# Optimization experiments

Measured on AMD Instinct MI355X. Metric: run time of the kernel, lower is better.

The kernel has to match this reference:

```python
import jax, jax.numpy as jnp
import numpy as np

B, S, D = 1, 2048, 2048
H = 16            # num query heads
QL = 1536         # q_lora_rank
KVL = 512         # kv_lora_rank
DN = 128          # qk_nope_head_dim
DR = 64           # qk_rope_head_dim
DV = 128          # v_head_dim
F = 8192          # ffn intermediate
EPS = 1e-6
WAVE = 10000.0


def _rms(x, scale, eps=EPS):
    # fp32 norm then cast back, matching DeepSeekV3_1RMSNorm
    x32 = x.astype(jnp.float32)
    ms = jnp.mean(x32 * x32, axis=-1, keepdims=True)
    return (x32 * jax.lax.rsqrt(ms + eps)).astype(x.dtype) * scale


def _rope_tables(seq_len, dim):
    inv_freq = 1.0 / (WAVE ** (jnp.arange(0, dim, 2, dtype=jnp.float32) / dim))
    t = jnp.arange(seq_len, dtype=jnp.float32)[:, None] * inv_freq[None, :]  # [S, dim/2]
    emb = jnp.concatenate([t, t], axis=-1)  # [S, dim]
    return jnp.cos(emb), jnp.sin(emb)


def _apply_rope(x, cos, sin):
    # x: [B, S, H, dr]; rotate-half convention
    half = x.shape[-1] // 2
    x1, x2 = x[..., :half], x[..., half:]
    rot = jnp.concatenate([-x2, x1], axis=-1)
    return x * cos[None, :, None, :] + rot * sin[None, :, None, :]


def setup_inputs() -> dict:
    key = jax.random.key(0)
    ks = jax.random.split(key, 12)
    w = lambda k, shp: (jax.random.normal(k, shp, dtype=jnp.float32) * 0.02)
    inp = {
        "hidden_states": jax.random.normal(ks[0], (B, S, D), dtype=jnp.float32),
        "attention_mask": jnp.broadcast_to(jnp.tril(jnp.ones((S, S), dtype=bool)), (B, S, S)),
        "pre_attn_scale": jnp.ones((D,), jnp.float32),
        "wqa": w(ks[1], (D, QL)),
        "q_norm_scale": jnp.ones((QL,), jnp.float32),
        "wqb": w(ks[2], (QL, H * (DN + DR))),
        "wkva": w(ks[3], (D, KVL + DR)),
        "kv_norm_scale": jnp.ones((KVL,), jnp.float32),
        "wkvb": w(ks[4], (KVL, H * (DN + DV))),
        "wo": w(ks[5], (H * DV, D)),
        "pre_ffn_scale": jnp.ones((D,), jnp.float32),
        "wg": w(ks[6], (D, F)),
        "bg": jnp.zeros((F,), jnp.float32),
        "wu": w(ks[7], (D, F)),
        "bu": jnp.zeros((F,), jnp.float32),
        "wd": w(ks[8], (F, D)),
        "bd": jnp.zeros((D,), jnp.float32),
    }
    return inp


def reference(hidden_states, attention_mask, pre_attn_scale, wqa, q_norm_scale, wqb,
              wkva, kv_norm_scale, wkvb, wo, pre_ffn_scale, wg, bg, wu, bu, wd, bd):
    x = hidden_states
    # --- pre-attention RMSNorm ---
    n = _rms(x, pre_attn_scale)
    # --- MLA attention ---
    q = (_rms(n @ wqa, q_norm_scale) @ wqb).reshape(B, S, H, DN + DR)
    q_nope, q_rope = q[..., :DN], q[..., DN:]
    kva = n @ wkva                              # [B,S,KVL+DR]
    c_kv, k_rope = kva[..., :KVL], kva[..., KVL:]
    kv = (_rms(c_kv, kv_norm_scale) @ wkvb).reshape(B, S, H, DN + DV)
    k_nope, v = kv[..., :DN], kv[..., DN:]
    cos, sin = _rope_tables(S, DR)
    q_rope = _apply_rope(q_rope, cos, sin)
    k_rope = _apply_rope(k_rope[:, :, None, :], cos, sin)  # [B,S,1,DR] shared across heads
    qf = jnp.concatenate([q_nope, q_rope], axis=-1)
    kf = jnp.concatenate([k_nope, jnp.broadcast_to(k_rope, (B, S, H, DR))], axis=-1)
    scale = 1.0 / float(np.sqrt(DN + DR))
    scores = jnp.einsum('bqhd,bkhd->bhqk', qf, kf) * scale
    scores = jnp.where(attention_mask[:, None, :, :], scores, jnp.float32(-1e9))
    probs = jax.nn.softmax(scores, axis=-1)
    attn = jnp.einsum('bhqk,bkhd->bqhd', probs, v).reshape(B, S, H * DV)
    x = x + attn @ wo                            # residual 1 (dropout=0)
    # --- pre-FFN RMSNorm + dense SwiGLU FFN ---
    n = _rms(x, pre_ffn_scale)
    ff = (jax.nn.silu(n @ wg + bg) * (n @ wu + bu)) @ wd + bd
    return x + ff                                # residual 2
```

## Files before the change

kernel.cpp:

```cpp
#include <hip/hip_runtime.h>
#include <hip/hip_bf16.h>
#include <stdint.h>

typedef unsigned short u16;
using f32x4  = __attribute__((ext_vector_type(4))) float;
using bf16x8 = __attribute__((ext_vector_type(8))) __bf16;
using u32x4  = __attribute__((ext_vector_type(4))) uint32_t;
using u16x4  = __attribute__((ext_vector_type(4))) unsigned short;
using u16x8  = __attribute__((ext_vector_type(8))) unsigned short;

#define S_LEN 2048
#define DM    2048
#define NH    16
#define QLR   1536
#define KVLR  512
#define DNOPE 128
#define DROPE 64
#define DVAL  128
#define FFD   8192

static __device__ __forceinline__ float bf2f(u16 u) {
    union { uint32_t i; float f; } v; v.i = ((uint32_t)u) << 16; return v.f;
}
static __device__ __forceinline__ u16 f2bf(float f) {
    union { float f; uint32_t i; } v; v.f = f;
    uint32_t x = v.i;
    return (u16)((x + 0x7FFF + ((x >> 16) & 1)) >> 16);
}
static __device__ __forceinline__ void gload16(const u16* g, const u16* l) {
    __builtin_amdgcn_global_load_lds(
        (const __attribute__((address_space(1))) void*)g,
        (__attribute__((address_space(3))) void*)l, 16, 0, 0);
}

struct TWJob { const float* src; u16* dst; int R, C, xt, start; };
struct TWJobs { TWJob j[4]; };

__global__ __launch_bounds__(256)
void transpose_all(TWJobs jobs)
{
    __shared__ __align__(16) u16 tile[64][68];
    const int bid = blockIdx.x;
    int e = 0;
#pragma unroll
    for (int i = 1; i < 4; ++i) e = (bid >= jobs.j[i].start) ? i : e;
    const float* src = jobs.j[e].src;
    u16* dst = jobs.j[e].dst;
    const int R = jobs.j[e].R, C = jobs.j[e].C;
    const int local = bid - jobs.j[e].start;
    const int c0 = (local % jobs.j[e].xt) * 64;
    const int r0 = (local / jobs.j[e].xt) * 64;
    const int t = threadIdx.x;
#pragma unroll
    for (int i = 0; i < 4; ++i) {
        int idx = i * 256 + t;
        int r = idx >> 4, c4 = idx & 15;
        float4 v = *reinterpret_cast<const float4*>(&src[(size_t)(r0 + r) * C + c0 + c4 * 4]);
        u16x4 b; b[0] = f2bf(v.x); b[1] = f2bf(v.y); b[2] = f2bf(v.z); b[3] = f2bf(v.w);
        *reinterpret_cast<u16x4*>(&tile[r][c4 * 4]) = b;
    }
    __syncthreads();
#pragma unroll
    for (int i = 0; i < 4; ++i) {
        int idx = i * 256 + t;
        int rr = idx >> 4, k4 = idx & 15;
        u16x4 o;
#pragma unroll
        for (int j = 0; j < 4; ++j) o[j] = tile[k4 * 4 + j][rr];
        *reinterpret_cast<u16x4*>(&dst[(size_t)(c0 + rr) * R + r0 + k4 * 4]) = o;
    }
}

__global__ __launch_bounds__(256)
void transpose_v(const u16* __restrict__ kv, u16* __restrict__ vt)
{
    __shared__ __align__(16) u16 tile[64][76];
    const int t = threadIdx.x;
    const int s0 = blockIdx.x * 64;
    const int d0 = blockIdx.y * 64;
    const int h  = blockIdx.z;
#pragma unroll
    for (int i = 0; i < 2; ++i) {
        int idx = i * 256 + t;
        int s = idx >> 3, c8 = idx & 7;
        u16x8 v = *reinterpret_cast<const u16x8*>(kv + (size_t)(s0 + s) * (NH * 256) + h * 256 + 128 + d0 + c8 * 8);
        u16x4 lo, hi;
#pragma unroll
        for (int j = 0; j < 4; ++j) { lo[j] = v[j]; hi[j] = v[4 + j]; }
        *reinterpret_cast<u16x4*>(&tile[s][c8 * 8])     = lo;
        *reinterpret_cast<u16x4*>(&tile[s][c8 * 8 + 4]) = hi;
    }
    __syncthreads();
#pragma unroll
    for (int i = 0; i < 4; ++i) {
        int idx = i * 256 + t;
        int d = idx >> 4, s4 = idx & 15;
        u16x4 o;
#pragma unroll
        for (int j = 0; j < 4; ++j) o[j] = tile[s4 * 4 + j][d];
        *reinterpret_cast<u16x4*>(&vt[(size_t)(h * 128 + d0 + d) * S_LEN + s0 + s4 * 4]) = o;
    }
}

template<bool IN_F32>
__global__ __launch_bounds__(256)
void rms_norm(const void* __restrict__ in, int in_stride, int width,
              const float* __restrict__ scale, u16* __restrict__ out, int out_stride)
{
    const int row = blockIdx.x;
    const int t = threadIdx.x;
    const float* inf = (const float*)in;
    const u16*   inb = (const u16*)in;
    float ss = 0.f;
    for (int c = t; c < width; c += 256) {
        float v = IN_F32 ? inf[(size_t)row * in_stride + c] : bf2f(inb[(size_t)row * in_stride + c]);
        ss += v * v;
    }
#pragma unroll
    for (int o = 32; o > 0; o >>= 1) ss += __shfl_xor(ss, o);
    __shared__ float red[4];
    if ((t & 63) == 0) red[t >> 6] = ss;
    __syncthreads();
    float inv = rsqrtf((red[0] + red[1] + red[2] + red[3]) / (float)width + 1e-6f);
    for (int c = t; c < width; c += 256) {
        float v = IN_F32 ? inf[(size_t)row * in_stride + c] : bf2f(inb[(size_t)row * in_stride + c]);
        out[(size_t)row * out_stride + c] = f2bf(v * inv * scale[c]);
    }
}

__global__ __launch_bounds__(256)
void rope_qk(u16* __restrict__ q, const float* __restrict__ kva, u16* __restrict__ kr)
{
    const int s = blockIdx.x;
    const int t = threadIdx.x;
    for (int idx = t; idx < 544; idx += 256) {
        int d = idx & 31;
        float invf = powf(10000.f, -(float)(2 * d) / 64.f);
        float ang = (float)s * invf;
        float cs = cosf(ang), sn = sinf(ang);
        if (idx < 512) {
            int hh = idx >> 5;
            u16* base = q + ((size_t)s * NH + hh) * 192 + 128;
            float x1 = bf2f(base[d]), x2 = bf2f(base[d + 32]);
            base[d]      = f2bf(x1 * cs - x2 * sn);
            base[d + 32] = f2bf(x2 * cs + x1 * sn);
        } else {
            const float* kb = kva + (size_t)s * 576 + 512;
            float x1 = kb[d], x2 = kb[d + 32];
            kr[(size_t)s * 64 + d]      = f2bf(x1 * cs - x2 * sn);
            kr[(size_t)s * 64 + d + 32] = f2bf(x2 * cs + x1 * sn);
        }
    }
}

__global__ __launch_bounds__(256)
void init_out(const float* __restrict__ x2, const float* __restrict__ bd,
              float* __restrict__ out, int total4, int N)
{
    int i = blockIdx.x * 256 + threadIdx.x;
    const int stride = gridDim.x * 256;
    for (; i < total4; i += stride) {
        float4 r = ((const float4*)x2)[i];
        int col = (i * 4) & (N - 1);
        float4 b = *reinterpret_cast<const float4*>(&bd[col]);
        float4 o; o.x = r.x + b.x; o.y = r.y + b.y; o.z = r.z + b.z; o.w = r.w + b.w;
        ((float4*)out)[i] = o;
    }
}

__global__ __launch_bounds__(256)
void mul_gu(const u16* __restrict__ g, const u16* __restrict__ u,
            u16* __restrict__ h, int total8)
{
    int i = blockIdx.x * 256 + threadIdx.x;
    const int stride = gridDim.x * 256;
    for (; i < total8; i += stride) {
        u16x8 gv = ((const u16x8*)g)[i];
        u16x8 uv = ((const u16x8*)u)[i];
        u16x8 hv;
#pragma unroll
        for (int j = 0; j < 8; ++j) hv[j] = f2bf(bf2f(gv[j]) * bf2f(uv[j]));
        ((u16x8*)h)[i] = hv;
    }
}

struct GJob { const u16* A; const u16* BT; void* out; int N, K, yCount, zCount; };

template<int EPI>
__global__ __launch_bounds__(256)
void gemm_bt2(GJob j0, GJob j1)
{
    __shared__ __align__(16) u16 As[128 * 64];
    __shared__ __align__(16) u16 Bs[128 * 64];
    const int t = threadIdx.x;
    const int lane = t & 63;
    const int w = t >> 6;
    const int wr = w >> 1, wc = w & 1;
    const int li = lane & 15;
    const int lg = lane >> 4;

    const int gx = gridDim.x;
    int nwg = gx * gridDim.y;
    int bid = blockIdx.y * gx + blockIdx.x;
    bid = (bid & 7) * (nwg >> 3) + (bid >> 3);
    const int m0 = (bid % gx) * 128;
    int yy = bid / gx;

    const int j0span = j0.yCount * j0.zCount;
    const GJob& J = (yy < j0span) ? j0 : j1;
    if (yy >= j0span) yy -= j0span;
    const int ntile = yy % J.yCount;
    const int z = yy / J.yCount;
    const int n0 = ntile * 128;
    const int N = J.N, K = J.K;

    const int nktt = K >> 6;
    const int nz = J.zCount;
    const int qq = nktt / nz, rr = nktt % nz;
    const int kt0 = z * qq + (z < rr ? z : rr);
    const int ktEnd = kt0 + qq + (z < rr ? 1 : 0);

    const int srow = w * 32 + (lane >> 3);
    const int scol = (((lane & 7) ^ (lane >> 3)) << 3);
    const u16* ag = J.A  + (size_t)(m0 + srow) * K + scol;
    const u16* bg = J.BT + (size_t)(n0 + srow) * K + scol;

    f32x4 acc[4][4];
#pragma unroll
    for (int m = 0; m < 4; ++m)
#pragma unroll
        for (int n = 0; n < 4; ++n)
            acc[m][n] = f32x4{0.f, 0.f, 0.f, 0.f};

    for (int kt = kt0; kt < ktEnd; ++kt) {
        const int k0 = kt << 6;
        __syncthreads();
#pragma unroll
        for (int i = 0; i < 4; ++i) {
            gload16(ag + (size_t)i * 8 * K + k0, As + (w * 32 + i * 8) * 64);
            gload16(bg + (size_t)i * 8 * K + k0, Bs + (w * 32 + i * 8) * 64);
        }
        __syncthreads();
#pragma unroll
        for (int kk = 0; kk < 2; ++kk) {
            const int csw = (kk * 32 + lg * 8) ^ ((li & 7) << 3);
            bf16x8 af[4], bfr[4];
#pragma unroll
            for (int m = 0; m < 4; ++m)
                af[m] = *reinterpret_cast<const bf16x8*>(As + (wr * 64 + m * 16 + li) * 64 + csw);
#pragma unroll
            for (int n = 0; n < 4; ++n)
                bfr[n] = *reinterpret_cast<const bf16x8*>(Bs + (wc * 64 + n * 16 + li) * 64 + csw);
#pragma unroll
            for (int m = 0; m < 4; ++m)
#pragma unroll
                for (int n = 0; n < 4; ++n)
                    acc[m][n] = __builtin_amdgcn_mfma_f32_16x16x32_bf16(af[m], bfr[n], acc[m][n], 0, 0, 0);
        }
    }

#pragma unroll
    for (int m = 0; m < 4; ++m) {
        const int row = m0 + wr * 64 + m * 16 + lg * 4;
#pragma unroll
        for (int n = 0; n < 4; ++n) {
            const int col = n0 + wc * 64 + n * 16 + li;
            if (col < N) {
#pragma unroll
                for (int r2 = 0; r2 < 4; ++r2) {
                    float v = acc[m][n][r2];
                    size_t idx = (size_t)(row + r2) * N + col;
                    if (EPI == 0) ((u16*)J.out)[idx] = f2bf(v);
                    else          unsafeAtomicAdd((float*)J.out + idx, v);
                }
            }
        }
    }
}

template<int EPI>
__global__ __launch_bounds__(512, 4)
void gemm_big(const u16* __restrict__ A, const u16* __restrict__ BT,
              void* __restrict__ out, int M, int N, int K,
              const float* __restrict__ bias, const u16* __restrict__ gmul)
{
    __shared__ __align__(16) u16 As[256 * 64];
    __shared__ __align__(16) u16 Bs[128 * 64];
    const int t = threadIdx.x;
    const int lane = t & 63;
    const int w = t >> 6;
    const int wr = w >> 1, wc = w & 1;
    const int li = lane & 15;
    const int lg = lane >> 4;

    const int gx = gridDim.x;
    int nwg = gx * gridDim.y;
    int bid = blockIdx.y * gx + blockIdx.x;
    bid = (bid & 7) * (nwg >> 3) + (bid >> 3);
    const int m0 = (bid % gx) * 256;
    const int n0 = (bid / gx) * 128;

    const int nz = gridDim.z, z = blockIdx.z;
    const int nktt = K >> 6;
    const int qq = nktt / nz, rr = nktt % nz;
    const int kt0 = z * qq + (z < rr ? z : rr);
    const int ktEnd = kt0 + qq + (z < rr ? 1 : 0);

    const int sr = lane >> 3;
    const int scol = (((lane & 7) ^ sr) << 3);
    const u16* ag = A  + (size_t)(m0 + w * 8 + sr) * K + scol;
    const u16* bg = BT + (size_t)(n0 + w * 8 + sr) * K + scol;
    const u16* lA = As + (w * 8) * 64;
    const u16* lB = Bs + (w * 8) * 64;

    f32x4 acc[4][4];
#pragma unroll
    for (int m = 0; m < 4; ++m)
#pragma unroll
        for (int n = 0; n < 4; ++n)
            acc[m][n] = f32x4{0.f, 0.f, 0.f, 0.f};

    for (int kt = kt0; kt < ktEnd; ++kt) {
        const int k0 = kt << 6;
        __syncthreads();
#pragma unroll
        for (int i = 0; i < 4; ++i)
            gload16(ag + (size_t)i * 64 * K + k0, lA + i * 64 * 64);
#pragma unroll
        for (int i = 0; i < 2; ++i)
            gload16(bg + (size_t)i * 64 * K + k0, lB + i * 64 * 64);
        __syncthreads();
        __builtin_amdgcn_s_setprio(1);
#pragma unroll
        for (int kk = 0; kk < 2; ++kk) {
            const int csw = (kk * 32 + lg * 8) ^ ((li & 7) << 3);
            bf16x8 af[4], bfr[4];
#pragma unroll
            for (int m = 0; m < 4; ++m)
                af[m] = *reinterpret_cast<const bf16x8*>(As + (wr * 64 + m * 16 + li) * 64 + csw);
#pragma unroll
            for (int n = 0; n < 4; ++n)
                bfr[n] = *reinterpret_cast<const bf16x8*>(Bs + (wc * 64 + n * 16 + li) * 64 + csw);
#pragma unroll
            for (int m = 0; m < 4; ++m)
#pragma unroll
                for (int n = 0; n < 4; ++n)
                    acc[m][n] = __builtin_amdgcn_mfma_f32_16x16x32_bf16(af[m], bfr[n], acc[m][n], 0, 0, 0);
        }
        __builtin_amdgcn_s_setprio(0);
    }

#pragma unroll
    for (int m = 0; m < 4; ++m) {
        const int row = m0 + wr * 64 + m * 16 + lg * 4;
#pragma unroll
        for (int n = 0; n < 4; ++n) {
            const int col = n0 + wc * 64 + n * 16 + li;
#pragma unroll
            for (int r2 = 0; r2 < 4; ++r2) {
                float v = acc[m][n][r2];
                size_t idx = (size_t)(row + r2) * N + col;
                if (EPI == 0) {
                    ((u16*)out)[idx] = f2bf(v);
                } else if (EPI == 1) {
                    v += bias[col];
                    v = v / (1.f + __expf(-v));
                    ((u16*)out)[idx] = f2bf(v);
                } else {
                    unsafeAtomicAdd((float*)out + idx, v);
                }
            }
        }
    }
}

__global__ __launch_bounds__(512, 4)
void gemm_gu(const u16* __restrict__ A, const u16* __restrict__ BgT, const u16* __restrict__ BuT,
             u16* __restrict__ gout, u16* __restrict__ uout, int M, int N, int K,
             const float* __restrict__ bg, const float* __restrict__ bu)
{
    __shared__ __align__(16) u16 As[256 * 64];
    __shared__ __align__(16) u16 Bs[128 * 64];
    const int t = threadIdx.x;
    const int lane = t & 63;
    const int w = t >> 6;
    const int wr = w >> 1, wc = w & 1;
    const int li = lane & 15;
    const int lg = lane >> 4;
    const int isUp = blockIdx.z;

    const u16* BT = isUp ? BuT : BgT;
    const float* bias = isUp ? bu : bg;
    u16* out = isUp ? uout : gout;

    const int gx = gridDim.x;
    int nwg = gx * gridDim.y;
    int bid = blockIdx.y * gx + blockIdx.x;
    bid = (bid & 7) * (nwg >> 3) + (bid >> 3);
    const int m0 = (bid % gx) * 256;
    const int n0 = (bid / gx) * 128;

    const int sr = lane >> 3;
    const int scol = (((lane & 7) ^ sr) << 3);
    const u16* ag = A  + (size_t)(m0 + w * 8 + sr) * K + scol;
    const u16* bgp = BT + (size_t)(n0 + w * 8 + sr) * K + scol;
    const u16* lA = As + (w * 8) * 64;
    const u16* lB = Bs + (w * 8) * 64;

    f32x4 acc[4][4];
#pragma unroll
    for (int m = 0; m < 4; ++m)
#pragma unroll
        for (int n = 0; n < 4; ++n)
            acc[m][n] = f32x4{0.f, 0.f, 0.f, 0.f};

    const int nkt = K >> 6;
    for (int kt = 0; kt < nkt; ++kt) {
        const int k0 = kt << 6;
        __syncthreads();
#pragma unroll
        for (int i = 0; i < 4; ++i)
            gload16(ag + (size_t)i * 64 * K + k0, lA + i * 64 * 64);
#pragma unroll
        for (int i = 0; i < 2; ++i)
            gload16(bgp + (size_t)i * 64 * K + k0, lB + i * 64 * 64);
        __syncthreads();
        __builtin_amdgcn_s_setprio(1);
#pragma unroll
        for (int kk = 0; kk < 2; ++kk) {
            const int csw = (kk * 32 + lg * 8) ^ ((li & 7) << 3);
            bf16x8 af[4], bfr[4];
#pragma unroll
            for (int m = 0; m < 4; ++m)
                af[m] = *reinterpret_cast<const bf16x8*>(As + (wr * 64 + m * 16 + li) * 64 + csw);
#pragma unroll
            for (int n = 0; n < 4; ++n)
                bfr[n] = *reinterpret_cast<const bf16x8*>(Bs + (wc * 64 + n * 16 + li) * 64 + csw);
#pragma unroll
            for (int m = 0; m < 4; ++m)
#pragma unroll
                for (int n = 0; n < 4; ++n)
                    acc[m][n] = __builtin_amdgcn_mfma_f32_16x16x32_bf16(af[m], bfr[n], acc[m][n], 0, 0, 0);
        }
        __builtin_amdgcn_s_setprio(0);
    }

#pragma unroll
    for (int m = 0; m < 4; ++m) {
        const int row = m0 + wr * 64 + m * 16 + lg * 4;
#pragma unroll
        for (int n = 0; n < 4; ++n) {
            const int col = n0 + wc * 64 + n * 16 + li;
            float bv = bias[col];
#pragma unroll
            for (int r2 = 0; r2 < 4; ++r2) {
                float v = acc[m][n][r2] + bv;
                if (!isUp) v = v / (1.f + __expf(-v));
                ((u16*)out)[(size_t)(row + r2) * N + col] = f2bf(v);
            }
        }
    }
}

struct TW4 { const float* src; u16* dst; int R, C, xt, gstart; };
struct TW4s { TW4 j[4]; };

__global__ __launch_bounds__(512)
void attn_tw(const u16* __restrict__ q, const u16* __restrict__ kv,
             const u16* __restrict__ kr, const u16* __restrict__ vt,
             u16* __restrict__ attn, TW4s tj)
{
    __shared__ __align__(16) u16 SMEM[2 * 20480 + 8 * 16 * 72];

    if (blockIdx.y >= 16) {
        u16 (*tile)[68] = reinterpret_cast<u16(*)[68]>(SMEM);
        const int g = (blockIdx.y - 16) * 16 + blockIdx.x;
        int e = 0;
#pragma unroll
        for (int i = 1; i < 4; ++i) e = (g >= tj.j[i].gstart) ? i : e;
        const float* src = tj.j[e].src;
        u16* dst = tj.j[e].dst;
        const int R = tj.j[e].R, C = tj.j[e].C, xt = tj.j[e].xt;
        const int base = (g - tj.j[e].gstart) * 8;
        const int t = threadIdx.x;
        for (int ti = 0; ti < 8; ++ti) {
            const int local = base + ti;
            const int c0 = (local % xt) * 64;
            const int r0 = (local / xt) * 64;
            __syncthreads();
#pragma unroll
            for (int i = 0; i < 2; ++i) {
                int idx = i * 512 + t;
                int r = idx >> 4, c4 = idx & 15;
                float4 v = *reinterpret_cast<const float4*>(&src[(size_t)(r0 + r) * C + c0 + c4 * 4]);
                u16x4 b; b[0] = f2bf(v.x); b[1] = f2bf(v.y); b[2] = f2bf(v.z); b[3] = f2bf(v.w);
                *reinterpret_cast<u16x4*>(&tile[r][c4 * 4]) = b;
            }
            __syncthreads();
#pragma unroll
            for (int i = 0; i < 2; ++i) {
                int idx = i * 512 + t;
                int rr = idx >> 4, k4 = idx & 15;
                u16x4 o;
#pragma unroll
                for (int j = 0; j < 4; ++j) o[j] = tile[k4 * 4 + j][rr];
                *reinterpret_cast<u16x4*>(&dst[(size_t)(c0 + rr) * R + r0 + k4 * 4]) = o;
            }
        }
        return;
    }

    u16 (*KVs)[20480] = reinterpret_cast<u16(*)[20480]>(SMEM);
    u16 (*Ps)[16][72] = reinterpret_cast<u16(*)[16][72]>(SMEM + 2 * 20480);

    const int t = threadIdx.x;
    const int lane = t & 63;
    const int w = t >> 6;
    const int li = lane & 15;
    const int lg = lane >> 4;
    const int h = blockIdx.x;
    const int b = 15 - blockIdx.y;

    const int qt = (w < 4) ? (2 * b + 1) : (2 * b);
    const int my_nkt = qt + 1;
    const int block_nkt = 2 * b + 2;
    const int wl = w & 3;
    const int qr = qt * 64 + wl * 16;
    const int qpos = qr + li;

    auto stage = [&](int buf, int k0) {
        u16* base = &KVs[buf][0];
#pragma unroll
        for (int i = 0; i < 3; ++i) {
            int g = w * 3 + i;
            int P = g * 64 + lane;
            int j = P / 24, s = P % 24;
            int c = (s & 24) | ((s ^ (j & 7)) & 7);
            const u16* src = (c < 16)
                ? kv + (size_t)(k0 + j) * (NH * 256) + h * 256 + c * 8
                : kr + (size_t)(k0 + j) * 64 + (c - 16) * 8;
            gload16(src, base + g * 512);
        }
#pragma unroll
        for (int i = 0; i < 2; ++i) {
            int g = w * 2 + i;
            int P = g * 64 + lane;
            int d = P >> 3, s8 = P & 7;
            int c = s8 ^ (d & 7);
            const u16* src = vt + (size_t)(h * 128 + d) * S_LEN + k0 + c * 8;
            gload16(src, base + 12288 + g * 512);
        }
    };

    bf16x8 qf[6];
#pragma unroll
    for (int kb = 0; kb < 6; ++kb)
        qf[kb] = *reinterpret_cast<const bf16x8*>(q + ((size_t)(qr + li) * NH + h) * 192 + kb * 32 + lg * 8);

    f32x4 oacc[8];
#pragma unroll
    for (int i = 0; i < 8; ++i) oacc[i] = f32x4{0.f, 0.f, 0.f, 0.f};
    float m_run = -INFINITY, l_run = 0.f;

    stage(0, 0);
    int buf = 0;
    const float scale = 0.07216878364870322f;

    for (int kt = 0; kt < block_nkt; ++kt) {
        const int k0 = kt << 6;
        __syncthreads();
        if (kt + 1 < block_nkt) stage(buf ^ 1, (kt + 1) << 6);

        if (kt < my_nkt) {
            const u16* bb = &KVs[buf][0];

            f32x4 sacc[4];
#pragma unroll
            for (int jt = 0; jt < 4; ++jt) sacc[jt] = f32x4{0.f, 0.f, 0.f, 0.f};
            __builtin_amdgcn_s_setprio(1);
#pragma unroll
            for (int kb = 0; kb < 6; ++kb) {
                const int c = kb * 4 + lg;
                const int s = (c & 24) | ((c ^ (li & 7)) & 7);
#pragma unroll
                for (int jt = 0; jt < 4; ++jt) {
                    bf16x8 kf = *reinterpret_cast<const bf16x8*>(bb + ((jt * 16 + li) * 24 + s) * 8);
                    sacc[jt] = __builtin_amdgcn_mfma_f32_16x16x32_bf16(kf, qf[kb], sacc[jt], 0, 0, 0);
                }
            }
            __builtin_amdgcn_s_setprio(0);

            float p[16];
            float mt = -INFINITY;
            if (k0 + 63 <= qr) {
#pragma unroll
                for (int jt = 0; jt < 4; ++jt)
#pragma unroll
                    for (int r = 0; r < 4; ++r) {
                        float sv = sacc[jt][r] * scale;
                        p[jt * 4 + r] = sv;
                        mt = fmaxf(mt, sv);
                    }
            } else {
#pragma unroll
                for (int jt = 0; jt < 4; ++jt)
#pragma unroll
                    for (int r = 0; r < 4; ++r) {
                        int jpos = k0 + jt * 16 + lg * 4 + r;
                        float sv = (jpos <= qpos) ? sacc[jt][r] * scale : -INFINITY;
                        p[jt * 4 + r] = sv;
                        mt = fmaxf(mt, sv);
                    }
            }
            mt = fmaxf(mt, __shfl_xor(mt, 16));
            mt = fmaxf(mt, __shfl_xor(mt, 32));
            if (!__all(mt <= m_run + 8.f)) {
                float mn = fmaxf(m_run, mt);
                float sf = __expf(m_run - mn);
                float sfr[4];
#pragma unroll
                for (int r = 0; r < 4; ++r)
                    sfr[r] = __shfl(sf, (lane & 48) + lg * 4 + r);
#pragma unroll
                for (int d2 = 0; d2 < 8; ++d2)
#pragma unroll
                    for (int r = 0; r < 4; ++r)
                        oacc[d2][r] *= sfr[r];
                l_run *= sf;
                m_run = mn;
            }
            float rsum = 0.f;
#pragma unroll
            for (int i2 = 0; i2 < 16; ++i2) { p[i2] = __expf(p[i2] - m_run); rsum += p[i2]; }
            rsum += __shfl_xor(rsum, 16);
            rsum += __shfl_xor(rsum, 32);
            l_run += rsum;

#pragma unroll
            for (int jt = 0; jt < 4; ++jt) {
                u16x4 pk;
                pk[0] = f2bf(p[jt * 4 + 0]); pk[1] = f2bf(p[jt * 4 + 1]);
                pk[2] = f2bf(p[jt * 4 + 2]); pk[3] = f2bf(p[jt * 4 + 3]);
                *reinterpret_cast<u16x4*>(&Ps[w][li][jt * 16 + lg * 4]) = pk;
            }

            __builtin_amdgcn_s_setprio(1);
#pragma unroll
            for (int ks = 0; ks < 2; ++ks) {
                bf16x8 pf = *reinterpret_cast<const bf16x8*>(&Ps[w][li][ks * 32 + lg * 8]);
                const int vs = (ks * 4 + lg) ^ (li & 7);
#pragma unroll
                for (int d2 = 0; d2 < 8; ++d2) {
                    bf16x8 vf = *reinterpret_cast<const bf16x8*>(bb + 12288 + ((d2 * 16 + li) * 8 + vs) * 8);
                    oacc[d2] = __builtin_amdgcn_mfma_f32_16x16x32_bf16(pf, vf, oacc[d2], 0, 0, 0);
                }
            }
            __builtin_amdgcn_s_setprio(0);
        }
        buf ^= 1;
    }

    float rl = 1.f / l_run;
    float rlr[4];
#pragma unroll
    for (int r = 0; r < 4; ++r)
        rlr[r] = __shfl(rl, (lane & 48) + lg * 4 + r);
#pragma unroll
    for (int d2 = 0; d2 < 8; ++d2)
#pragma unroll
        for (int r = 0; r < 4; ++r) {
            int srow = qr + lg * 4 + r;
            int dcol = d2 * 16 + li;
            attn[(size_t)srow * (NH * DVAL) + h * DVAL + dcol] = f2bf(oacc[d2][r] * rlr[r]);
        }
}

extern "C" void kernel_launch(void* const* d_in, const int* in_sizes, int n_in,
                              void* d_out, int out_size, void* d_ws, size_t ws_size,
                              hipStream_t stream)
{
    const float* hidden   = (const float*)d_in[0];
    const float* pa_scale = (const float*)d_in[2];
    const float* wqa      = (const float*)d_in[3];
    const float* qn_scale = (const float*)d_in[4];
    const float* wqb      = (const float*)d_in[5];
    const float* wkva     = (const float*)d_in[6];
    const float* kv_scale = (const float*)d_in[7];
    const float* wkvb     = (const float*)d_in[8];
    const float* wo       = (const float*)d_in[9];
    const float* pf_scale = (const float*)d_in[10];
    const float* wg       = (const float*)d_in[11];
    const float* bg       = (const float*)d_in[12];
    const float* wu       = (const float*)d_in[13];
    const float* bu       = (const float*)d_in[14];
    const float* wd       = (const float*)d_in[15];
    const float* bd       = (const float*)d_in[16];
    float* out = (float*)d_out;

    size_t off = 0;
    auto alloc = [&](size_t bytes) {
        off = (off + 255) & ~(size_t)255;
        void* p = (char*)d_ws + off;
        off += bytes;
        return p;
    };
    u16* wqaT  = (u16*)alloc((size_t)QLR * DM * 2);
    u16* wqbT  = (u16*)alloc((size_t)3072 * QLR * 2);
    u16* wkvaT = (u16*)alloc((size_t)640 * DM * 2);
    u16* wkvbT = (u16*)alloc((size_t)4096 * KVLR * 2);
    u16* woT   = (u16*)alloc((size_t)DM * DM * 2);
    u16* wgT   = (u16*)alloc((size_t)FFD * DM * 2);
    u16* wuT   = (u16*)alloc((size_t)FFD * DM * 2);
    u16* wdT   = (u16*)alloc((size_t)DM * FFD * 2);
    u16* n1    = (u16*)alloc((size_t)S_LEN * DM * 2);
    float* qlora32 = (float*)alloc((size_t)S_LEN * QLR * 4);
    float* kva32   = (float*)alloc((size_t)S_LEN * 576 * 4);
    u16* qn    = (u16*)alloc((size_t)S_LEN * QLR * 2);
    u16* qbuf  = (u16*)alloc((size_t)S_LEN * 3072 * 2);
    u16* ckvn  = (u16*)alloc((size_t)S_LEN * KVLR * 2);
    u16* kvbuf = (u16*)alloc((size_t)S_LEN * 4096 * 2);
    u16* krbuf = (u16*)alloc((size_t)S_LEN * 64 * 2);
    u16* attnb = (u16*)alloc((size_t)S_LEN * DM * 2);
    float* x2  = (float*)alloc((size_t)S_LEN * DM * 4);
    u16* n2    = (u16*)alloc((size_t)S_LEN * DM * 2);
    u16* gbuf  = (u16*)alloc((size_t)S_LEN * FFD * 2);
    u16* hbuf  = (u16*)alloc((size_t)S_LEN * FFD * 2);
    u16* vtb  = (u16*)qlora32;
    u16* ubuf = (u16*)qlora32;
    (void)ws_size; (void)in_sizes; (void)n_in; (void)out_size;

    TWJobs ejobs;
    int startAcc = 0;
    auto setE = [&](int i, const float* s, u16* d, int R, int C) {
        ejobs.j[i] = TWJob{s, d, R, C, C / 64, startAcc};
        startAcc += (C / 64) * (R / 64);
    };
    setE(0, wqa,  wqaT,  2048, 1536);
    setE(1, wqb,  wqbT,  1536, 3072);
    setE(2, wkva, wkvaT, 2048,  576);
    setE(3, wkvb, wkvbT,  512, 4096);
    hipLaunchKernelGGL(transpose_all, dim3(startAcc), 256, 0, stream, ejobs);

    hipMemsetAsync(qlora32, 0, (size_t)S_LEN * QLR * 4, stream);
    hipMemsetAsync(kva32,   0, (size_t)S_LEN * 576 * 4, stream);

    hipLaunchKernelGGL((rms_norm<true>),  dim3(S_LEN), 256, 0, stream, hidden, DM, DM, pa_scale, n1, DM);

    {
        GJob jqa  {n1, wqaT,  qlora32, QLR, DM, 12, 2};
        GJob jkva {n1, wkvaT, kva32,   576, DM,  5, 4};
        hipLaunchKernelGGL((gemm_bt2<5>), dim3(16, 44), 256, 0, stream, jqa, jkva);
    }
    hipLaunchKernelGGL((rms_norm<true>), dim3(S_LEN), 256, 0, stream, qlora32, QLR, QLR, qn_scale, qn, QLR);
    hipLaunchKernelGGL((rms_norm<true>), dim3(S_LEN), 256, 0, stream, kva32, 576, KVLR, kv_scale, ckvn, KVLR);
    {
        GJob jqb  {qn,   wqbT,  qbuf,  3072, QLR,  24, 1};
        GJob jkvb {ckvn, wkvbT, kvbuf, 4096, KVLR, 32, 1};
        hipLaunchKernelGGL((gemm_bt2<0>), dim3(16, 56), 256, 0, stream, jqb, jkvb);
    }
    hipLaunchKernelGGL(rope_qk, dim3(S_LEN), 256, 0, stream, qbuf, kva32, krbuf);

    hipLaunchKernelGGL(transpose_v, dim3(S_LEN/64, 2, NH), 256, 0, stream, kvbuf, vtb);

    TW4s tj;
    int gAcc = 0;
    auto setL = [&](int i, const float* s, u16* d, int R, int C) {
        tj.j[i] = TW4{s, d, R, C, C / 64, gAcc};
        gAcc += (C / 64) * (R / 64) / 8;
    };
    setL(0, wo, woT, 2048, 2048);
    setL(1, wg, wgT, 2048, 8192);
    setL(2, wu, wuT, 2048, 8192);
    setL(3, wd, wdT, 8192, 2048);
    hipLaunchKernelGGL(attn_tw, dim3(16, 16 + 104), 512, 0, stream, qbuf, kvbuf, krbuf, vtb, attnb, tj);

    hipMemcpyAsync(x2, hidden, (size_t)S_LEN * DM * 4, hipMemcpyDeviceToDevice, stream);
    hipLaunchKernelGGL((gemm_big<5>), dim3(8, 16, 4), 512, 0, stream, attnb, woT, x2, S_LEN, DM, DM, nullptr, nullptr);

    hipLaunchKernelGGL((rms_norm<true>), dim3(S_LEN), 256, 0, stream, x2, DM, DM, pf_scale, n2, DM);

    hipLaunchKernelGGL(init_out, dim3(2048), 256, 0, stream, x2, bd, out, S_LEN * DM / 4, DM);
    hipLaunchKernelGGL(gemm_gu, dim3(8, 64, 2), 512, 0, stream, n2, wgT, wuT, gbuf, ubuf, S_LEN, FFD, DM, bg, bu);
    hipLaunchKernelGGL(mul_gu, dim3(2048), 256, 0, stream, gbuf, ubuf, hbuf, S_LEN * FFD / 8);
    hipLaunchKernelGGL((gemm_big<5>), dim3(8, 16, 4), 512, 0, stream, hbuf, wdT, out, S_LEN, DM, FFD, nullptr, nullptr);
}
```

Measured before the change: 625.8 us.

## Merge small kernels and move q/kv-b projections to big-tile GEMM

Fuses the two post-LoRA RMSNorms into one launch, merges rope and V-transpose into a single kernel, and folds the init_out bias/residual copy into extra blocks of the gate/up GEMM. The q_b and kv_b projections move from the 256-thread gemm_bt2 to a new two-job 256x128-tile gemm_big2. The aim is to cut launch overhead and raise GEMM tile efficiency. In exchange, gemm_gu gets a tail row of memory-bound blocks, and the larger tiles give fewer workgroups for the small-K kv_b GEMM.

```diff
diff --git a/kernel.cpp b/kernel.cpp
--- a/kernel.cpp
+++ b/kernel.cpp
@@ -71,37 +71,6 @@
     }
 }
 
-__global__ __launch_bounds__(256)
-void transpose_v(const u16* __restrict__ kv, u16* __restrict__ vt)
-{
-    __shared__ __align__(16) u16 tile[64][76];
-    const int t = threadIdx.x;
-    const int s0 = blockIdx.x * 64;
-    const int d0 = blockIdx.y * 64;
-    const int h  = blockIdx.z;
-#pragma unroll
-    for (int i = 0; i < 2; ++i) {
-        int idx = i * 256 + t;
-        int s = idx >> 3, c8 = idx & 7;
-        u16x8 v = *reinterpret_cast<const u16x8*>(kv + (size_t)(s0 + s) * (NH * 256) + h * 256 + 128 + d0 + c8 * 8);
-        u16x4 lo, hi;
-#pragma unroll
-        for (int j = 0; j < 4; ++j) { lo[j] = v[j]; hi[j] = v[4 + j]; }
-        *reinterpret_cast<u16x4*>(&tile[s][c8 * 8])     = lo;
-        *reinterpret_cast<u16x4*>(&tile[s][c8 * 8 + 4]) = hi;
-    }
-    __syncthreads();
-#pragma unroll
-    for (int i = 0; i < 4; ++i) {
-        int idx = i * 256 + t;
-        int d = idx >> 4, s4 = idx & 15;
-        u16x4 o;
-#pragma unroll
-        for (int j = 0; j < 4; ++j) o[j] = tile[s4 * 4 + j][d];
-        *reinterpret_cast<u16x4*>(&vt[(size_t)(h * 128 + d0 + d) * S_LEN + s0 + s4 * 4]) = o;
-    }
-}
-
 template<bool IN_F32>
 __global__ __launch_bounds__(256)
 void rms_norm(const void* __restrict__ in, int in_stride, int width,
@@ -129,42 +98,89 @@
 }
 
 __global__ __launch_bounds__(256)
-void rope_qk(u16* __restrict__ q, const float* __restrict__ kva, u16* __restrict__ kr)
-{
-    const int s = blockIdx.x;
+void rms_norm2(const float* __restrict__ inA, int strideA, int widthA,
+               const float* __restrict__ scaleA, u16* __restrict__ outA, int ostrA,
+               const float* __restrict__ inB, int strideB, int widthB,
+               const float* __restrict__ scaleB, u16* __restrict__ outB, int ostrB)
+{
+    const float* in   = blockIdx.y ? inB : inA;
+    const float* scale= blockIdx.y ? scaleB : scaleA;
+    u16* out          = blockIdx.y ? outB : outA;
+    const int stride  = blockIdx.y ? strideB : strideA;
+    const int width   = blockIdx.y ? widthB : widthA;
+    const int ostr    = blockIdx.y ? ostrB : ostrA;
+    const int row = blockIdx.x;
     const int t = threadIdx.x;
-    for (int idx = t; idx < 544; idx += 256) {
-        int d = idx & 31;
-        float invf = powf(10000.f, -(float)(2 * d) / 64.f);
-        float ang = (float)s * invf;
-        float cs = cosf(ang), sn = sinf(ang);
-        if (idx < 512) {
-            int hh = idx >> 5;
-            u16* base = q + ((size_t)s * NH + hh) * 192 + 128;
-            float x1 = bf2f(base[d]), x2 = bf2f(base[d + 32]);
-            base[d]      = f2bf(x1 * cs - x2 * sn);
-            base[d + 32] = f2bf(x2 * cs + x1 * sn);
-        } else {
-            const float* kb = kva + (size_t)s * 576 + 512;
-            float x1 = kb[d], x2 = kb[d + 32];
-            kr[(size_t)s * 64 + d]      = f2bf(x1 * cs - x2 * sn);
-            kr[(size_t)s * 64 + d + 32] = f2bf(x2 * cs + x1 * sn);
-        }
+    float ss = 0.f;
+    for (int c = t; c < width; c += 256) {
+        float v = in[(size_t)row * stride + c];
+        ss += v * v;
+    }
+#pragma unroll
+    for (int o = 32; o > 0; o >>= 1) ss += __shfl_xor(ss, o);
+    __shared__ float red[4];
+    if ((t & 63) == 0) red[t >> 6] = ss;
+    __syncthreads();
+    float inv = rsqrtf((red[0] + red[1] + red[2] + red[3]) / (float)width + 1e-6f);
+    for (int c = t; c < width; c += 256) {
+        float v = in[(size_t)row * stride + c];
+        out[(size_t)row * ostr + c] = f2bf(v * inv * scale[c]);
     }
 }
 
 __global__ __launch_bounds__(256)
-void init_out(const float* __restrict__ x2, const float* __restrict__ bd,
-              float* __restrict__ out, int total4, int N)
-{
-    int i = blockIdx.x * 256 + threadIdx.x;
-    const int stride = gridDim.x * 256;
-    for (; i < total4; i += stride) {
-        float4 r = ((const float4*)x2)[i];
-        int col = (i * 4) & (N - 1);
-        float4 b = *reinterpret_cast<const float4*>(&bd[col]);
-        float4 o; o.x = r.x + b.x; o.y = r.y + b.y; o.z = r.z + b.z; o.w = r.w + b.w;
-        ((float4*)out)[i] = o;
+void rope_tv(u16* __restrict__ q, const float* __restrict__ kva, u16* __restrict__ kr,
+             const u16* __restrict__ kv, u16* __restrict__ vt)
+{
+    const int bid = blockIdx.x;
+    const int t = threadIdx.x;
+    if (bid < S_LEN) {
+        const int s = bid;
+        for (int idx = t; idx < 544; idx += 256) {
+            int d = idx & 31;
+            float invf = powf(10000.f, -(float)(2 * d) / 64.f);
+            float ang = (float)s * invf;
+            float cs = cosf(ang), sn = sinf(ang);
+            if (idx < 512) {
+                int hh = idx >> 5;
+                u16* base = q + ((size_t)s * NH + hh) * 192 + 128;
+                float x1 = bf2f(base[d]), x2 = bf2f(base[d + 32]);
+                base[d]      = f2bf(x1 * cs - x2 * sn);
+                base[d + 32] = f2bf(x2 * cs + x1 * sn);
+            } else {
+                const float* kb = kva + (size_t)s * 576 + 512;
+                float x1 = kb[d], x2 = kb[d + 32];
+                kr[(size_t)s * 64 + d]      = f2bf(x1 * cs - x2 * sn);
+                kr[(size_t)s * 64 + d + 32] = f2bf(x2 * cs + x1 * sn);
+            }
+        }
+        return;
+    }
+    __shared__ __align__(16) u16 tile[64][76];
+    const int t2 = bid - S_LEN;
+    const int s0 = (t2 & 31) * 64;
+    const int d0 = ((t2 >> 5) & 1) * 64;
+    const int h  = t2 >> 6;
+#pragma unroll
+    for (int i = 0; i < 2; ++i) {
+        int idx = i * 256 + t;
+        int s = idx >> 3, c8 = idx & 7;
+        u16x8 v = *reinterpret_cast<const u16x8*>(kv + (size_t)(s0 + s) * (NH * 256) + h * 256 + 128 + d0 + c8 * 8);
+        u16x4 lo, hi;
+#pragma unroll
+        for (int j = 0; j < 4; ++j) { lo[j] = v[j]; hi[j] = v[4 + j]; }
+        *reinterpret_cast<u16x4*>(&tile[s][c8 * 8])     = lo;
+        *reinterpret_cast<u16x4*>(&tile[s][c8 * 8 + 4]) = hi;
+    }
+    __syncthreads();
+#pragma unroll
+    for (int i = 0; i < 4; ++i) {
+        int idx = i * 256 + t;
+        int d = idx >> 4, s4 = idx & 15;
+        u16x4 o;
+#pragma unroll
+        for (int j = 0; j < 4; ++j) o[j] = tile[s4 * 4 + j][d];
+        *reinterpret_cast<u16x4*>(&vt[(size_t)(h * 128 + d0 + d) * S_LEN + s0 + s4 * 4]) = o;
     }
 }
 
@@ -278,11 +294,10 @@
     }
 }
 
-template<int EPI>
+struct BJob { const u16* A; const u16* BT; u16* out; int N, K, yCount; };
+
 __global__ __launch_bounds__(512, 4)
-void gemm_big(const u16* __restrict__ A, const u16* __restrict__ BT,
-              void* __restrict__ out, int M, int N, int K,
-              const float* __restrict__ bias, const u16* __restrict__ gmul)
+void gemm_big2(BJob j0, BJob j1)
 {
     __shared__ __align__(16) u16 As[256 * 64];
     __shared__ __align__(16) u16 Bs[128 * 64];
@@ -298,18 +313,17 @@
     int bid = blockIdx.y * gx + blockIdx.x;
     bid = (bid & 7) * (nwg >> 3) + (bid >> 3);
     const int m0 = (bid % gx) * 256;
-    const int n0 = (bid / gx) * 128;
-
-    const int nz = gridDim.z, z = blockIdx.z;
-    const int nktt = K >> 6;
-    const int qq = nktt / nz, rr = nktt % nz;
-    const int kt0 = z * qq + (z < rr ? z : rr);
-    const int ktEnd = kt0 + qq + (z < rr ? 1 : 0);
+    int yy = bid / gx;
+
+    const BJob& J = (yy < j0.yCount) ? j0 : j1;
+    if (yy >= j0.yCount) yy -= j0.yCount;
+    const int n0 = yy * 128;
+    const int N = J.N, K = J.K;
 
     const int sr = lane >> 3;
     const int scol = (((lane & 7) ^ sr) << 3);
-    const u16* ag = A  + (size_t)(m0 + w * 8 + sr) * K + scol;
-    const u16* bg = BT + (size_t)(n0 + w * 8 + sr) * K + scol;
+    const u16* ag = J.A  + (size_t)(m0 + w * 8 + sr) * K + scol;
+    const u16* bg = J.BT + (size_t)(n0 + w * 8 + sr) * K + scol;
     const u16* lA = As + (w * 8) * 64;
     const u16* lB = Bs + (w * 8) * 64;
 
@@ -320,7 +334,8 @@
         for (int n = 0; n < 4; ++n)
             acc[m][n] = f32x4{0.f, 0.f, 0.f, 0.f};
 
-    for (int kt = kt0; kt < ktEnd; ++kt) {
+    const int nkt = K >> 6;
+    for (int kt = 0; kt < nkt; ++kt) {
         const int k0 = kt << 6;
         __syncthreads();
 #pragma unroll
@@ -357,27 +372,17 @@
         for (int n = 0; n < 4; ++n) {
             const int col = n0 + wc * 64 + n * 16 + li;
 #pragma unroll
-            for (int r2 = 0; r2 < 4; ++r2) {
-                float v = acc[m][n][r2];
-                size_t idx = (size_t)(row + r2) * N + col;
-                if (EPI == 0) {
-                    ((u16*)out)[idx] = f2bf(v);
-                } else if (EPI == 1) {
-                    v += bias[col];
-                    v = v / (1.f + __expf(-v));
-                    ((u16*)out)[idx] = f2bf(v);
-                } else {
-                    unsafeAtomicAdd((float*)out + idx, v);
-                }
-            }
-        }
-    }
-}
-
+            for (int r2 = 0; r2 < 4; ++r2)
+                J.out[(size_t)(row + r2) * N + col] = f2bf(acc[m][n][r2]);
+        }
+    }
+}
+
+template<int EPI>
 __global__ __launch_bounds__(512, 4)
-void gemm_gu(const u16* __restrict__ A, const u16* __restrict__ BgT, const u16* __restrict__ BuT,
-             u16* __restrict__ gout, u16* __restrict__ uout, int M, int N, int K,
-             const float* __restrict__ bg, const float* __restrict__ bu)
+void gemm_big(const u16* __restrict__ A, const u16* __restrict__ BT,
+              void* __restrict__ out, int M, int N, int K,
+              const float* __restrict__ bias, const u16* __restrict__ gmul)
 {
     __shared__ __align__(16) u16 As[256 * 64];
     __shared__ __align__(16) u16 Bs[128 * 64];
@@ -387,11 +392,6 @@
     const int wr = w >> 1, wc = w & 1;
     const int li = lane & 15;
     const int lg = lane >> 4;
-    const int isUp = blockIdx.z;
-
-    const u16* BT = isUp ? BuT : BgT;
-    const float* bias = isUp ? bu : bg;
-    u16* out = isUp ? uout : gout;
 
     const int gx = gridDim.x;
     int nwg = gx * gridDim.y;
@@ -400,6 +400,116 @@
     const int m0 = (bid % gx) * 256;
     const int n0 = (bid / gx) * 128;
 
+    const int nz = gridDim.z, z = blockIdx.z;
+    const int nktt = K >> 6;
+    const int qq = nktt / nz, rr = nktt % nz;
+    const int kt0 = z * qq + (z < rr ? z : rr);
+    const int ktEnd = kt0 + qq + (z < rr ? 1 : 0);
+
+    const int sr = lane >> 3;
+    const int scol = (((lane & 7) ^ sr) << 3);
+    const u16* ag = A  + (size_t)(m0 + w * 8 + sr) * K + scol;
+    const u16* bg = BT + (size_t)(n0 + w * 8 + sr) * K + scol;
+    const u16* lA = As + (w * 8) * 64;
+    const u16* lB = Bs + (w * 8) * 64;
+
+    f32x4 acc[4][4];
+#pragma unroll
+    for (int m = 0; m < 4; ++m)
+#pragma unroll
+        for (int n = 0; n < 4; ++n)
+            acc[m][n] = f32x4{0.f, 0.f, 0.f, 0.f};
+
+    for (int kt = kt0; kt < ktEnd; ++kt) {
+        const int k0 = kt << 6;
+        __syncthreads();
+#pragma unroll
+        for (int i = 0; i < 4; ++i)
+            gload16(ag + (size_t)i * 64 * K + k0, lA + i * 64 * 64);
+#pragma unroll
+        for (int i = 0; i < 2; ++i)
+            gload16(bg + (size_t)i * 64 * K + k0, lB + i * 64 * 64);
+        __syncthreads();
+        __builtin_amdgcn_s_setprio(1);
+#pragma unroll
+        for (int kk = 0; kk < 2; ++kk) {
+            const int csw = (kk * 32 + lg * 8) ^ ((li & 7) << 3);
+            bf16x8 af[4], bfr[4];
+#pragma unroll
+            for (int m = 0; m < 4; ++m)
+                af[m] = *reinterpret_cast<const bf16x8*>(As + (wr * 64 + m * 16 + li) * 64 + csw);
+#pragma unroll
+            for (int n = 0; n < 4; ++n)
+                bfr[n] = *reinterpret_cast<const bf16x8*>(Bs + (wc * 64 + n * 16 + li) * 64 + csw);
+#pragma unroll
+            for (int m = 0; m < 4; ++m)
+#pragma unroll
+                for (int n = 0; n < 4; ++n)
+                    acc[m][n] = __builtin_amdgcn_mfma_f32_16x16x32_bf16(af[m], bfr[n], acc[m][n], 0, 0, 0);
+        }
+        __builtin_amdgcn_s_setprio(0);
+    }
+
+#pragma unroll
+    for (int m = 0; m < 4; ++m) {
+        const int row = m0 + wr * 64 + m * 16 + lg * 4;
+#pragma unroll
+        for (int n = 0; n < 4; ++n) {
+            const int col = n0 + wc * 64 + n * 16 + li;
+#pragma unroll
+            for (int r2 = 0; r2 < 4; ++r2) {
+                float v = acc[m][n][r2];
+                size_t idx = (size_t)(row + r2) * N + col;
+                if (EPI == 0) ((u16*)out)[idx] = f2bf(v);
+                else          unsafeAtomicAdd((float*)out + idx, v);
+            }
+        }
+    }
+}
+
+__global__ __launch_bounds__(512, 4)
+void gemm_gu(const u16* __restrict__ A, const u16* __restrict__ BgT, const u16* __restrict__ BuT,
+             u16* __restrict__ gout, u16* __restrict__ uout, int M, int N, int K,
+             const float* __restrict__ bg, const float* __restrict__ bu,
+             const float* __restrict__ x2i, const float* __restrict__ bdi, float* __restrict__ outi)
+{
+    const int isUp = blockIdx.z;
+    if (blockIdx.y == gridDim.y - 1) {
+        const int total4 = S_LEN * DM / 4;
+        const int half = total4 / 2;
+        int i = isUp * half + blockIdx.x * 512 + threadIdx.x;
+        const int end = isUp * half + half;
+        const int stride = gridDim.x * 512;
+        for (; i < end; i += stride) {
+            float4 r = ((const float4*)x2i)[i];
+            int col = (i * 4) & (DM - 1);
+            float4 b = *reinterpret_cast<const float4*>(&bdi[col]);
+            float4 o; o.x = r.x + b.x; o.y = r.y + b.y; o.z = r.z + b.z; o.w = r.w + b.w;
+            ((float4*)outi)[i] = o;
+        }
+        return;
+    }
+
+    __shared__ __align__(16) u16 As[256 * 64];
+    __shared__ __align__(16) u16 Bs[128 * 64];
+    const int t = threadIdx.x;
+    const int lane = t & 63;
+    const int w = t >> 6;
+    const int wr = w >> 1, wc = w & 1;
+    const int li = lane & 15;
+    const int lg = lane >> 4;
+
+    const u16* BT = isUp ? BuT : BgT;
+    const float* bias = isUp ? bu : bg;
+    u16* out = isUp ? uout : gout;
+
+    const int gx = gridDim.x;
+    int nwg = gx * (gridDim.y - 1);
+    int bid = blockIdx.y * gx + blockIdx.x;
+    bid = (bid & 7) * (nwg >> 3) + (bid >> 3);
+    const int m0 = (bid % gx) * 256;
+    const int n0 = (bid / gx) * 128;
+
     const int sr = lane >> 3;
     const int scol = (((lane & 7) ^ sr) << 3);
     const u16* ag = A  + (size_t)(m0 + w * 8 + sr) * K + scol;
@@ -456,7 +566,7 @@
             for (int r2 = 0; r2 < 4; ++r2) {
                 float v = acc[m][n][r2] + bv;
                 if (!isUp) v = v / (1.f + __expf(-v));
-                ((u16*)out)[(size_t)(row + r2) * N + col] = f2bf(v);
+                out[(size_t)(row + r2) * N + col] = f2bf(v);
             }
         }
     }
@@ -751,16 +861,15 @@
         GJob jkva {n1, wkvaT, kva32,   576, DM,  5, 4};
         hipLaunchKernelGGL((gemm_bt2<5>), dim3(16, 44), 256, 0, stream, jqa, jkva);
     }
-    hipLaunchKernelGGL((rms_norm<true>), dim3(S_LEN), 256, 0, stream, qlora32, QLR, QLR, qn_scale, qn, QLR);
-    hipLaunchKernelGGL((rms_norm<true>), dim3(S_LEN), 256, 0, stream, kva32, 576, KVLR, kv_scale, ckvn, KVLR);
+    hipLaunchKernelGGL(rms_norm2, dim3(S_LEN, 2), 256, 0, stream,
+                       qlora32, QLR, QLR, qn_scale, qn, QLR,
+                       kva32, 576, KVLR, kv_scale, ckvn, KVLR);
     {
-        GJob jqb  {qn,   wqbT,  qbuf,  3072, QLR,  24, 1};
-        GJob jkvb {ckvn, wkvbT, kvbuf, 4096, KVLR, 32, 1};
-        hipLaunchKernelGGL((gemm_bt2<0>), dim3(16, 56), 256, 0, stream, jqb, jkvb);
-    }
-    hipLaunchKernelGGL(rope_qk, dim3(S_LEN), 256, 0, stream, qbuf, kva32, krbuf);
-
-    hipLaunchKernelGGL(transpose_v, dim3(S_LEN/64, 2, NH), 256, 0, stream, kvbuf, vtb);
+        BJob jqb  {qn,   wqbT,  qbuf,  3072, QLR,  24};
+        BJob jkvb {ckvn, wkvbT, kvbuf, 4096, KVLR, 32};
+        hipLaunchKernelGGL(gemm_big2, dim3(8, 56), 512, 0, stream, jqb, jkvb);
+    }
+    hipLaunchKernelGGL(rope_tv, dim3(S_LEN + 1024), 256, 0, stream, qbuf, kva32, krbuf, kvbuf, vtb);
 
     TW4s tj;
     int gAcc = 0;
@@ -779,8 +888,8 @@
 
     hipLaunchKernelGGL((rms_norm<true>), dim3(S_LEN), 256, 0, stream, x2, DM, DM, pf_scale, n2, DM);
 
-    hipLaunchKernelGGL(init_out, dim3(2048), 256, 0, stream, x2, bd, out, S_LEN * DM / 4, DM);
-    hipLaunchKernelGGL(gemm_gu, dim3(8, 64, 2), 512, 0, stream, n2, wgT, wuT, gbuf, ubuf, S_LEN, FFD, DM, bg, bu);
+    hipLaunchKernelGGL(gemm_gu, dim3(8, 65, 2), 512, 0, stream, n2, wgT, wuT, gbuf, ubuf,
+                       S_LEN, FFD, DM, bg, bu, x2, bd, out);
     hipLaunchKernelGGL(mul_gu, dim3(2048), 256, 0, stream, gbuf, ubuf, hbuf, S_LEN * FFD / 8);
     hipLaunchKernelGGL((gemm_big<5>), dim3(8, 16, 4), 512, 0, stream, hbuf, wdT, out, S_LEN, DM, FFD, nullptr, nullptr);
 }
```

Measured after the change: 627.6 us. No clear change (+0.3%).
